# Kernel tuning notes

Hardware: AMD Instinct MI355X
Metric: run time of the kernel (lower is better)

The kernel has to match this reference:

```python
import jax, jax.numpy as jnp
import numpy as np

MAX_SIGMA = 10.0
TRUNCATE = 4.0
R = int(TRUNCATE * MAX_SIGMA + 0.5)  # 40, static max radius (scipy: int(truncate*sigma+0.5))
L = 2 * R + 1                         # 81


def _make_kernels(sigmas):
    # sigmas: [B] -> kernels [B, L], exactly matching scipy._gaussian_kernel1d
    pos = jnp.arange(-R, R + 1, dtype=sigmas.dtype)          # [L]
    r = jnp.floor(TRUNCATE * sigmas + 0.5)                   # per-sample radius
    w = jnp.exp(-0.5 * (pos[None, :] ** 2) / (sigmas[:, None] ** 2))
    w = w * (jnp.abs(pos)[None, :] <= r[:, None])            # scipy truncation
    return w / jnp.sum(w, axis=-1, keepdims=True)


def _reflect_index(n):
    # symmetric ('reflect' in scipy) boundary indices for pad width R, valid even if R > n
    i = jnp.arange(-R, n + R)
    j = jnp.mod(i, 2 * n)
    return jnp.where(j < n, j, 2 * n - 1 - j)


def _conv_last(x, k):
    # correlate along last axis with reflect boundary; x [..., n], k [L]
    n = x.shape[-1]
    xp = x[..., _reflect_index(n)]                            # [..., n+2R]
    flat = xp.reshape(-1, 1, n + 2 * R)
    out = jax.lax.conv_general_dilated(flat, k[None, None, :],
                                       window_strides=(1,), padding='VALID')
    return out.reshape(x.shape)


def _blur_one(xi, k):
    # xi: [C, H, W]; scipy gaussian_filter with scalar sigma blurs every axis
    for ax in range(xi.ndim):
        xi = jnp.moveaxis(_conv_last(jnp.moveaxis(xi, ax, -1), k), -1, ax)
    return xi


def setup_inputs() -> dict:
    key = jax.random.key(0)
    k1, _ = jax.random.split(key)
    B, C, H, W = 64, 3, 512, 512
    x = jax.random.uniform(k1, (B, C, H, W), dtype=jnp.float32)
    blur_sigmas = jnp.asarray(np.geomspace(0.5, MAX_SIGMA, 10), dtype=jnp.float32)
    fwd_steps = jax.random.randint(jax.random.fold_in(key, 1), (B,), 0, 10, dtype=jnp.int32)
    return {"x": x, "blur_sigmas": blur_sigmas, "fwd_steps": fwd_steps}


def reference(x, blur_sigmas, fwd_steps):
    sigmas = blur_sigmas[fwd_steps]          # [B]
    kernels = _make_kernels(sigmas)          # [B, L]
    return jax.vmap(_blur_one)(x, kernels)   # [B, C, H, W]
```

## Files before the change

### kernel.cpp

```cpp
#include <hip/hip_runtime.h>
#include <hip/hip_bf16.h>

#define RMAX 40
#define LK   81
#define HH   512
#define WW   512
#define CC   3
#define BB   64
#define ROWS 2
#define TH   32

typedef unsigned short u16;

__device__ __forceinline__ u16 f2bf(float f) {
    unsigned u = __float_as_uint(f);
    u += 0x7FFFu + ((u >> 16) & 1u);
    return (u16)(u >> 16);
}
__device__ __forceinline__ float bf2f(u16 s) {
    return __uint_as_float(((unsigned)s) << 16);
}

__global__ void prep_kernel(const float* __restrict__ sigmas10,
                            const int* __restrict__ steps,
                            int* __restrict__ rbuf,
                            float* __restrict__ mbuf,
                            float* __restrict__ wbuf)
{
    int b = threadIdx.x;
    if (b >= BB) return;
    float sigma = sigmas10[steps[b]];
    int r = (int)floorf(4.0f * sigma + 0.5f);
    if (r > RMAX) r = RMAX;
    float s2 = sigma * sigma;

    float sum = 0.0f;
    for (int p = -r; p <= r; ++p)
        sum += expf(-0.5f * (float)(p * p) / s2);
    float inv = 1.0f / sum;

    for (int i = 0; i < 128; ++i) wbuf[b * 128 + i] = 0.0f;
    for (int p = -r; p <= r; ++p)
        wbuf[b * 128 + 16 + (p + RMAX)] = expf(-0.5f * (float)(p * p) / s2) * inv;

    float Mm[9];
    for (int i = 0; i < 9; ++i) Mm[i] = 0.0f;
    for (int p = -r; p <= r; ++p) {
        float wv = expf(-0.5f * (float)(p * p) / s2) * inv;
        for (int c = 0; c < CC; ++c) {
            int i = c + p;
            int j = ((i % 6) + 6) % 6;
            int cc = (j < 3) ? j : 5 - j;
            Mm[c * 3 + cc] += wv;
        }
    }
    for (int c = 0; c < 3; ++c)
        for (int cc = 0; cc < 3; ++cc)
            mbuf[b * 12 + c * 4 + cc] = Mm[c * 3 + cc];
    rbuf[b] = r;
}

__global__ __launch_bounds__(256) void passB_kernel(
    const float* __restrict__ x,
    const float* __restrict__ wbuf,
    const float* __restrict__ mbuf,
    const int*   __restrict__ rbuf,
    u16* __restrict__ out1)
{
    __shared__ __align__(16) float mixed[CC * ROWS][WW + 2 * RMAX];

    const int b   = blockIdx.y;
    const int h0  = blockIdx.x * ROWS;
    const int tid = threadIdx.x;
    const int r   = __builtin_amdgcn_readfirstlane(rbuf[b]);

    const float M00 = mbuf[b * 12 + 0], M01 = mbuf[b * 12 + 1], M02 = mbuf[b * 12 + 2];
    const float M10 = mbuf[b * 12 + 4], M11 = mbuf[b * 12 + 5], M12 = mbuf[b * 12 + 6];
    const float M20 = mbuf[b * 12 + 8], M21 = mbuf[b * 12 + 9], M22 = mbuf[b * 12 + 10];

    const float* xb = x + (size_t)b * CC * HH * WW + (size_t)h0 * WW;

    for (int idx = tid; idx < WW + 2 * RMAX; idx += 256) {
        int i  = idx - RMAX;
        int jm = i & (2 * WW - 1);
        int src = (jm < WW) ? jm : (2 * WW - 1 - jm);
        float a0 = __builtin_nontemporal_load(xb + src);
        float a1 = __builtin_nontemporal_load(xb + HH * WW + src);
        float a2 = __builtin_nontemporal_load(xb + 2 * HH * WW + src);
        float b0 = __builtin_nontemporal_load(xb + WW + src);
        float b1 = __builtin_nontemporal_load(xb + HH * WW + WW + src);
        float b2 = __builtin_nontemporal_load(xb + 2 * HH * WW + WW + src);
        mixed[0][idx] = M00 * a0 + M01 * a1 + M02 * a2;
        mixed[1][idx] = M00 * b0 + M01 * b1 + M02 * b2;
        mixed[2][idx] = M10 * a0 + M11 * a1 + M12 * a2;
        mixed[3][idx] = M10 * b0 + M11 * b1 + M12 * b2;
        mixed[4][idx] = M20 * a0 + M21 * a1 + M22 * a2;
        mixed[5][idx] = M20 * b0 + M21 * b1 + M22 * b2;
    }
    __syncthreads();

    const int t0    = (RMAX - r) & ~3;
    const int n4    = ((r + RMAX + 3 - t0) >> 2) + 1;
    const int kbase = (16 + t0) >> 2;
    const float4* K4 = (const float4*)(wbuf + b * 128);

#pragma unroll
    for (int k = 0; k < 3; ++k) {
        const int task = tid + 256 * k;
        const int g    = task & 127;
        const int rc   = task >> 7;
        const int w0   = g << 2;

        const int dbase = (w0 + t0) >> 2;
        const float4* D4 = (const float4*)(&mixed[rc][0]);

        float4 Wlo = K4[kbase - 1];
        float acc0 = 0.f, acc1 = 0.f, acc2 = 0.f, acc3 = 0.f;

        for (int s = 0; s < n4; ++s) {
            float4 Whi = K4[kbase + s];
            float4 D   = D4[dbase + s];
            acc0 += Whi.x * D.x; acc1 += Wlo.w * D.x; acc2 += Wlo.z * D.x; acc3 += Wlo.y * D.x;
            acc0 += Whi.y * D.y; acc1 += Whi.x * D.y; acc2 += Wlo.w * D.y; acc3 += Wlo.z * D.y;
            acc0 += Whi.z * D.z; acc1 += Whi.y * D.z; acc2 += Whi.x * D.z; acc3 += Wlo.w * D.z;
            acc0 += Whi.w * D.w; acc1 += Whi.z * D.w; acc2 += Whi.y * D.w; acc3 += Whi.x * D.w;
            Wlo = Whi;
        }

        ushort4 o;
        o.x = f2bf(acc0); o.y = f2bf(acc1); o.z = f2bf(acc2); o.w = f2bf(acc3);
        const int c = rc >> 1, row = rc & 1;
        u16* dst = out1 + ((size_t)b * CC + c) * HH * WW
                 + (size_t)(h0 + row) * WW + w0;
        *(ushort4*)dst = o;
    }
}

__device__ __forceinline__ int refl512(int i) {
    int jm = i & (2 * HH - 1);
    return (jm < HH) ? jm : (2 * HH - 1 - jm);
}

__global__ __launch_bounds__(256) void passC_kernel(
    const u16* __restrict__ in1,
    const float* __restrict__ wbuf,
    const int*   __restrict__ rbuf,
    float* __restrict__ out)
{
    const int tid = threadIdx.x;
    const int w   = blockIdx.x * 256 + tid;
    const int h0  = blockIdx.y * TH;
    const int bc  = blockIdx.z;
    const int b   = bc / 3;
    const int r   = __builtin_amdgcn_readfirstlane(rbuf[b]);

    const u16*  src = in1 + (size_t)bc * HH * WW;
    const float* kw  = wbuf + b * 128;

    float acc[TH];
    float D[TH];
#pragma unroll
    for (int j = 0; j < TH; ++j) acc[j] = 0.0f;

#pragma unroll
    for (int q = 0; q < TH; ++q)
        D[q] = bf2f(src[(size_t)refl512(h0 - r + q) * WW + w]);

    const int Mr = (2 * r + TH) & ~(TH - 1);

    for (int c0 = 0; c0 < Mr; c0 += TH) {
#pragma unroll
        for (int u = 0; u < TH; ++u) {
            int m = c0 + u;
            float wgt = kw[16 + RMAX - r + m];
#pragma unroll
            for (int j = 0; j < TH; ++j)
                acc[j] += wgt * D[(u + j) & (TH - 1)];
            D[u] = bf2f(src[(size_t)refl512(h0 - r + m + TH) * WW + w]);
        }
    }

    float* dst = out + (size_t)bc * HH * WW + (size_t)h0 * WW + w;
#pragma unroll
    for (int j = 0; j < TH; ++j)
        __builtin_nontemporal_store(acc[j], dst + (size_t)j * WW);
}

extern "C" void kernel_launch(void* const* d_in, const int* in_sizes, int n_in,
                              void* d_out, int out_size, void* d_ws, size_t ws_size,
                              hipStream_t stream)
{
    const float* x      = (const float*)d_in[0];
    const float* sigmas = (const float*)d_in[1];
    const int*   steps  = (const int*)d_in[2];
    float*       out    = (float*)d_out;

    int*   rbuf  = (int*)d_ws;
    float* mbuf  = (float*)((char*)d_ws + 256);
    float* wbuf  = (float*)((char*)d_ws + 4096);
    u16*   inter = (u16*)((char*)d_ws + 65536);

    prep_kernel<<<1, 64, 0, stream>>>(sigmas, steps, rbuf, mbuf, wbuf);

    dim3 gB(HH / ROWS, BB);
    passB_kernel<<<gB, 256, 0, stream>>>(x, wbuf, mbuf, rbuf, inter);

    dim3 gC(WW / 256, HH / TH, BB * CC);
    passC_kernel<<<gC, 256, 0, stream>>>(inter, wbuf, rbuf, out);
}
```

Measured before the change: 423.6 us.

## Run vertical blur pass on MFMA with split-bf16 Toeplitz weight tables

Replaces the scalar FMA vertical convolution in passC with bf16 MFMA 16x16x32 instructions. The prep kernel now runs one block per sample and builds Toeplitz-structured weight fragments split into hi and lo bf16 parts to keep near-fp32 weight precision. Each wave computes 32 output rows for 16 columns using two accumulators over chunks of 32 taps. This targets the ALU-bound vertical pass but adds doubled MFMA work for the lo part and strided 2-byte gathers per lane.

```diff
diff --git a/kernel.cpp b/kernel.cpp
--- a/kernel.cpp
+++ b/kernel.cpp
@@ -8,9 +8,10 @@
 #define CC   3
 #define BB   64
 #define ROWS 2
-#define TH   32
 
 typedef unsigned short u16;
+typedef __attribute__((ext_vector_type(8))) short short8;
+typedef __attribute__((ext_vector_type(4))) float f32x4;
 
 __device__ __forceinline__ u16 f2bf(float f) {
     unsigned u = __float_as_uint(f);
@@ -21,43 +22,72 @@
     return __uint_as_float(((unsigned)s) << 16);
 }
 
-__global__ void prep_kernel(const float* __restrict__ sigmas10,
-                            const int* __restrict__ steps,
-                            int* __restrict__ rbuf,
-                            float* __restrict__ mbuf,
-                            float* __restrict__ wbuf)
-{
-    int b = threadIdx.x;
-    if (b >= BB) return;
-    float sigma = sigmas10[steps[b]];
+__global__ __launch_bounds__(256) void prep_kernel(
+    const float* __restrict__ sigmas10,
+    const int*   __restrict__ steps,
+    int*   __restrict__ rbuf,
+    float* __restrict__ mbuf,
+    float* __restrict__ wbuf,
+    u16*   __restrict__ atab)
+{
+    const int b   = blockIdx.x;
+    const int tid = threadIdx.x;
+    const float sigma = sigmas10[steps[b]];
     int r = (int)floorf(4.0f * sigma + 0.5f);
     if (r > RMAX) r = RMAX;
-    float s2 = sigma * sigma;
+    const float s2 = sigma * sigma;
 
     float sum = 0.0f;
     for (int p = -r; p <= r; ++p)
         sum += expf(-0.5f * (float)(p * p) / s2);
-    float inv = 1.0f / sum;
-
-    for (int i = 0; i < 128; ++i) wbuf[b * 128 + i] = 0.0f;
-    for (int p = -r; p <= r; ++p)
-        wbuf[b * 128 + 16 + (p + RMAX)] = expf(-0.5f * (float)(p * p) / s2) * inv;
-
-    float Mm[9];
-    for (int i = 0; i < 9; ++i) Mm[i] = 0.0f;
-    for (int p = -r; p <= r; ++p) {
-        float wv = expf(-0.5f * (float)(p * p) / s2) * inv;
-        for (int c = 0; c < CC; ++c) {
-            int i = c + p;
-            int j = ((i % 6) + 6) % 6;
-            int cc = (j < 3) ? j : 5 - j;
-            Mm[c * 3 + cc] += wv;
-        }
-    }
-    for (int c = 0; c < 3; ++c)
-        for (int cc = 0; cc < 3; ++cc)
-            mbuf[b * 12 + c * 4 + cc] = Mm[c * 3 + cc];
-    rbuf[b] = r;
+    const float inv = 1.0f / sum;
+
+    if (tid < 128) {
+        int p = tid - 56;
+        float v = 0.0f;
+        if (p >= -r && p <= r)
+            v = expf(-0.5f * (float)(p * p) / s2) * inv;
+        wbuf[b * 128 + tid] = v;
+    }
+
+    if (tid == 0) {
+        rbuf[b] = r;
+        float Mm[9];
+        for (int i = 0; i < 9; ++i) Mm[i] = 0.0f;
+        for (int p = -r; p <= r; ++p) {
+            float wv = expf(-0.5f * (float)(p * p) / s2) * inv;
+            for (int c = 0; c < CC; ++c) {
+                int i = c + p;
+                int j = ((i % 6) + 6) % 6;
+                int cc = (j < 3) ? j : 5 - j;
+                Mm[c * 3 + cc] += wv;
+            }
+        }
+        for (int c = 0; c < 3; ++c)
+            for (int cc = 0; cc < 3; ++cc)
+                mbuf[b * 12 + c * 4 + cc] = Mm[c * 3 + cc];
+    }
+
+    u16* ab = atab + (size_t)b * 8192;
+    int e = tid * 32;
+    for (int ee = 0; ee < 32; ++ee, ++e) {
+        int j    = e & 7;
+        int lane = (e >> 3) & 63;
+        int s    = e >> 9;
+        int ch   = s >> 2;
+        int half = (s >> 1) & 1;
+        int prec = s & 1;
+        int m = 32 * ch + ((lane >> 4) << 3) + j - (lane & 15) - 16 * half;
+        float wfull = 0.0f;
+        if (m >= 0 && m <= 2 * r) {
+            int p = m - r;
+            wfull = expf(-0.5f * (float)(p * p) / s2) * inv;
+        }
+        u16 hi = f2bf(wfull);
+        u16 val = hi;
+        if (prec) val = f2bf(wfull - bf2f(hi));
+        ab[e] = val;
+    }
 }
 
 __global__ __launch_bounds__(256) void passB_kernel(
@@ -143,47 +173,51 @@
 
 __global__ __launch_bounds__(256) void passC_kernel(
     const u16* __restrict__ in1,
-    const float* __restrict__ wbuf,
-    const int*   __restrict__ rbuf,
+    const u16* __restrict__ atab,
+    const int* __restrict__ rbuf,
     float* __restrict__ out)
 {
-    const int tid = threadIdx.x;
-    const int w   = blockIdx.x * 256 + tid;
-    const int h0  = blockIdx.y * TH;
-    const int bc  = blockIdx.z;
-    const int b   = bc / 3;
-    const int r   = __builtin_amdgcn_readfirstlane(rbuf[b]);
-
-    const u16*  src = in1 + (size_t)bc * HH * WW;
-    const float* kw  = wbuf + b * 128;
-
-    float acc[TH];
-    float D[TH];
+    const int tid  = threadIdx.x;
+    const int lane = tid & 63;
+    const int bc   = blockIdx.z;
+    const int b    = bc / 3;
+    const int r    = __builtin_amdgcn_readfirstlane(rbuf[b]);
+    const int h0   = blockIdx.y * 32;
+    const int w    = blockIdx.x * 64 + (tid >> 6) * 16 + (lane & 15);
+    const int nch  = (2 * r + 63) >> 5;
+    const int rowbase = h0 - r + ((lane >> 4) << 3);
+
+    const u16* src = in1 + (size_t)bc * HH * WW + w;
+    const short8* at = (const short8*)(atab + (size_t)b * 8192);
+
+    f32x4 acc0 = {0.f, 0.f, 0.f, 0.f};
+    f32x4 acc1 = {0.f, 0.f, 0.f, 0.f};
+
+    for (int ch = 0; ch < nch; ++ch) {
+        short8 bv;
 #pragma unroll
-    for (int j = 0; j < TH; ++j) acc[j] = 0.0f;
-
+        for (int j = 0; j < 8; ++j) {
+            int row = refl512(rowbase + 32 * ch + j);
+            bv[j] = (short)src[(size_t)row * WW];
+        }
+        short8 ah0 = at[(ch * 4 + 0) * 64 + lane];
+        short8 al0 = at[(ch * 4 + 1) * 64 + lane];
+        short8 ah1 = at[(ch * 4 + 2) * 64 + lane];
+        short8 al1 = at[(ch * 4 + 3) * 64 + lane];
+
+        acc0 = __builtin_amdgcn_mfma_f32_16x16x32_bf16(ah0, bv, acc0, 0, 0, 0);
+        acc0 = __builtin_amdgcn_mfma_f32_16x16x32_bf16(al0, bv, acc0, 0, 0, 0);
+        acc1 = __builtin_amdgcn_mfma_f32_16x16x32_bf16(ah1, bv, acc1, 0, 0, 0);
+        acc1 = __builtin_amdgcn_mfma_f32_16x16x32_bf16(al1, bv, acc1, 0, 0, 0);
+    }
+
+    const int orow = h0 + ((lane >> 4) << 2);
+    float* dst = out + (size_t)bc * HH * WW + (size_t)orow * WW + w;
 #pragma unroll
-    for (int q = 0; q < TH; ++q)
-        D[q] = bf2f(src[(size_t)refl512(h0 - r + q) * WW + w]);
-
-    const int Mr = (2 * r + TH) & ~(TH - 1);
-
-    for (int c0 = 0; c0 < Mr; c0 += TH) {
-#pragma unroll
-        for (int u = 0; u < TH; ++u) {
-            int m = c0 + u;
-            float wgt = kw[16 + RMAX - r + m];
-#pragma unroll
-            for (int j = 0; j < TH; ++j)
-                acc[j] += wgt * D[(u + j) & (TH - 1)];
-            D[u] = bf2f(src[(size_t)refl512(h0 - r + m + TH) * WW + w]);
-        }
-    }
-
-    float* dst = out + (size_t)bc * HH * WW + (size_t)h0 * WW + w;
-#pragma unroll
-    for (int j = 0; j < TH; ++j)
-        __builtin_nontemporal_store(acc[j], dst + (size_t)j * WW);
+    for (int q = 0; q < 4; ++q) {
+        __builtin_nontemporal_store(acc0[q], dst + (size_t)q * WW);
+        __builtin_nontemporal_store(acc1[q], dst + (size_t)(q + 16) * WW);
+    }
 }
 
 extern "C" void kernel_launch(void* const* d_in, const int* in_sizes, int n_in,
@@ -198,13 +232,14 @@
     int*   rbuf  = (int*)d_ws;
     float* mbuf  = (float*)((char*)d_ws + 256);
     float* wbuf  = (float*)((char*)d_ws + 4096);
-    u16*   inter = (u16*)((char*)d_ws + 65536);
-
-    prep_kernel<<<1, 64, 0, stream>>>(sigmas, steps, rbuf, mbuf, wbuf);
+    u16*   atab  = (u16*)((char*)d_ws + 65536);
+    u16*   inter = (u16*)((char*)d_ws + 65536 + (1 << 20));
+
+    prep_kernel<<<64, 256, 0, stream>>>(sigmas, steps, rbuf, mbuf, wbuf, atab);
 
     dim3 gB(HH / ROWS, BB);
     passB_kernel<<<gB, 256, 0, stream>>>(x, wbuf, mbuf, rbuf, inter);
 
-    dim3 gC(WW / 256, HH / TH, BB * CC);
-    passC_kernel<<<gC, 256, 0, stream>>>(inter, wbuf, rbuf, out);
-}
+    dim3 gC(WW / 64, HH / 32, BB * CC);
+    passC_kernel<<<gC, 256, 0, stream>>>(inter, atab, rbuf, out);
+}
```

New measurement: 409.8 us. 1.03x faster.
